# Optimization experiments

Measured on AMD Instinct MI355X. Metric: run time of the kernel, lower is better.

Reference implementation:

```python
import jax, jax.numpy as jnp
import numpy as np

# ---- constants from module defaults (n_transducers reduced 64->32) ----
ARC = 160          # transducer_arc_width
NTR = 32           # n_transducers
NMEAS = 256
NX = 360           # padded grid size
DX = 0.6
NSTEPS = 640       # nt
DT = 0.2
SIGMA = 12.0
TC = 3.2
FC = 1.0
NBC = 15
PAD = 73
C1, C2, C3 = -2.5, 4.0 / 3.0, -1.0 / 12.0

_thetas = np.linspace(0.0, 2.0 * np.pi, NMEAS + 1)[:-1]
_ti = np.floor(ARC * np.stack((np.cos(_thetas), np.sin(_thetas))) + (NX - 1) / 2).astype(np.int32)
MEAS_INDS = jnp.asarray(NX * _ti[0, :] + _ti[1, :])          # [256] flat grid indices
IN_INDS = MEAS_INDS[:: NMEAS // NTR]                         # [32] source-injection indices
_t = np.arange(NSTEPS) * DT
SOURCE = jnp.asarray((np.exp(-((_t - TC) ** 2) / (2.0 * SIGMA ** 2)) * np.sin(2.0 * np.pi * FC * _t)).astype(np.float32))


def get_abc(vp):
    # vp: [B, NX, NX] -> sponge damping profile, same overwrite order as torch code
    B = vp.shape[0]
    dimr = jnp.arange(NBC, dtype=vp.dtype)                   # [nbc]
    velmin = jnp.min(vp.reshape(B, -1), axis=-1)             # [B]
    a = (NBC - 1) * DX
    kappa = 3.0 * velmin * jnp.asarray(np.log(10000.0), vp.dtype) / (2.0 * a)
    d1 = kappa[:, None] * (dimr[None, :] * DX / a) ** 2      # [B, nbc]
    rev = d1[:, ::-1]
    damp = jnp.zeros_like(vp)
    damp = damp.at[:, :NBC, :].set(rev[:, :, None])
    damp = damp.at[:, -NBC:, :].set(d1[:, :, None])
    damp = damp.at[:, :, :NBC].set(rev[:, None, :])          # columns overwrite corners, as in torch
    damp = damp.at[:, :, -NBC:].set(d1[:, None, :])
    return damp


def _forward(v):
    v = jnp.pad(v[:, 0], ((0, 0), (PAD, PAD), (PAD, PAD)), constant_values=1.5)  # [B,360,360]
    B = v.shape[0]
    kappa = get_abc(v) * DT
    v2 = v * v
    alpha = v2 * (DT / DX) ** 2                              # [B,360,360]
    beta = (DT * DT) * v2.reshape(B, -1)[:, IN_INDS]         # [B,NTR]
    temp1 = 2.0 + 2.0 * C1 * alpha - kappa
    temp0 = 1.0 - kappa
    a_, t1_, t0_ = alpha[:, None], temp1[:, None], temp0[:, None]  # broadcast over transducer axis
    tx = jnp.arange(NTR)

    def step(carry, src_t):
        p0, p1 = carry                                        # each [B,NTR,360,360]
        lap = C2 * (jnp.roll(p1, 1, -2) + jnp.roll(p1, -1, -2) + jnp.roll(p1, 1, -1) + jnp.roll(p1, -1, -1)) \
            + C3 * (jnp.roll(p1, 2, -2) + jnp.roll(p1, -2, -2) + jnp.roll(p1, 2, -1) + jnp.roll(p1, -2, -1))
        p = a_ * lap + t1_ * p1 - t0_ * p0
        pf = p.reshape(B, NTR, NX * NX)
        pf = pf.at[:, tx, IN_INDS].add(beta * src_t)          # per-shot source injection
        m = pf[:, :, MEAS_INDS]                               # [B,NTR,NMEAS]
        return (p1, pf.reshape(B, NTR, NX, NX)), m

    z = jnp.zeros((B, NTR, NX, NX), dtype=v.dtype)
    _, meas = jax.lax.scan(step, (z, z), SOURCE)              # meas: [NSTEPS,B,NTR,NMEAS]
    return jnp.transpose(meas, (1, 2, 0, 3))                  # [B,NTR,NSTEPS,NMEAS]


def setup_inputs() -> dict:
    key = jax.random.key(0)
    v = jax.random.uniform(key, (1, 1, 214, 214), dtype=jnp.float32) + 1.0  # speeds ~[1,2]
    return {"v": v}


def reference(v):
    return _forward(v)
```

## Files before the change

kernel.cpp:

```cpp
#include <hip/hip_runtime.h>
#include <math.h>

#ifndef M_PI
#define M_PI 3.14159265358979323846
#endif

#define NXx   360
#define NXY   (NXx*NXx)
#define NTRc  32
#define NMEASc 256
#define NSTEPSc 640
#define NBCc  15
#define PADc  73
#define NVc   214

#define BROWS 45
#define NBANDS 8
#define NBLK  (NTRc*NBANDS)
#define NTHREADS 1024
#define NGrow (NXx/4)
#define GPB   (BROWS*NGrow)
#define NEDGE (4*NGrow)
#define LDSROWS 49
#define LDSFLOATS (2*LDSROWS*NXx)
#define NSLOT 4
#define HALO_PER (NSLOT*4*NXx)

#define C2f   1.3333334f
#define C3f  (-0.083333336f)
#define ADX2  0.11111111f
#define DT2f  0.04f
#define DTf   0.2f
#define DXf   0.6f

typedef float f32x4 __attribute__((ext_vector_type(4)));

__device__ __forceinline__ void store4_sys(float* p, float4 v) {
    f32x4 vv; vv.x = v.x; vv.y = v.y; vv.z = v.z; vv.w = v.w;
    asm volatile("global_store_dwordx4 %0, %1, off sc0 sc1" :: "v"(p), "v"(vv) : "memory");
}
__device__ __forceinline__ float4 load4_sys(const float* p) {
    f32x4 r;
    asm volatile("global_load_dwordx4 %0, %1, off sc0 sc1\n\ts_waitcnt vmcnt(0)"
                 : "=&v"(r) : "v"(p) : "memory");
    return make_float4(r.x, r.y, r.z, r.w);
}
__device__ __forceinline__ void storei_sys(int* p, int v) {
    asm volatile("global_store_dword %0, %1, off sc0 sc1" :: "v"(p), "v"(v) : "memory");
}
__device__ __forceinline__ int loadi_sys(const int* p) {
    int r;
    asm volatile("global_load_dword %0, %1, off sc0 sc1\n\ts_waitcnt vmcnt(0)"
                 : "=&v"(r) : "v"(p) : "memory");
    return r;
}
__device__ __forceinline__ void drain_vm() {
    asm volatile("s_waitcnt vmcnt(0)" ::: "memory");
}

__global__ void velmin_kernel(const float* __restrict__ v, float* __restrict__ velmin) {
    __shared__ float s[256];
    float m = 1.5f;
    for (int i = threadIdx.x; i < NVc*NVc; i += 256) m = fminf(m, v[i]);
    s[threadIdx.x] = m;
    __syncthreads();
    for (int o = 128; o > 0; o >>= 1) {
        if (threadIdx.x < o) s[threadIdx.x] = fminf(s[threadIdx.x], s[threadIdx.x+o]);
        __syncthreads();
    }
    if (threadIdx.x == 0) *velmin = s[0];
}

__global__ void coef_kernel(const float* __restrict__ v, const float* __restrict__ velmin_p,
                            float* __restrict__ alpha, float* __restrict__ kap) {
    int idx = blockIdx.x*256 + threadIdx.x;
    if (idx >= NXY) return;
    int i = idx / NXx, j = idx - i*NXx;
    float vc = 1.5f;
    if (i >= PADc && i < PADc+NVc && j >= PADc && j < PADc+NVc)
        vc = v[(i-PADc)*NVc + (j-PADc)];
    float v2 = vc*vc;
    float al = v2 * ADX2;
    float velmin = *velmin_p;
    const float a = (float)((NBCc-1)*0.6);
    float ks = 3.0f*velmin*9.2103405f/(2.0f*a);
    float damp = 0.0f;
    int k = -1;
    if (j >= NXx-NBCc)      k = j-(NXx-NBCc);
    else if (j < NBCc)      k = NBCc-1-j;
    else if (i >= NXx-NBCc) k = i-(NXx-NBCc);
    else if (i < NBCc)      k = NBCc-1-i;
    if (k >= 0) { float r = (float)k*DXf/a; damp = ks*r*r; }
    alpha[idx] = al;
    kap[idx]   = damp*DTf;
}

__global__ void beta_kernel(const float* __restrict__ v, const int* __restrict__ in_inds,
                            float* __restrict__ beta) {
    int tr = threadIdx.x;
    if (tr >= NTRc) return;
    int idx = in_inds[tr];
    int i = idx / NXx, j = idx - i*NXx;
    float vc = 1.5f;
    if (i >= PADc && i < PADc+NVc && j >= PADc && j < PADc+NVc)
        vc = v[(i-PADc)*NVc + (j-PADc)];
    beta[tr] = DT2f*vc*vc;
}

__global__ __launch_bounds__(NTHREADS, 4) void persist_kernel(
    const float* __restrict__ alpha, const float* __restrict__ kap,
    const float* __restrict__ beta, const float* __restrict__ src,
    const int* __restrict__ meas_inds, const int* __restrict__ in_inds,
    int* flags, float* haloG, float* __restrict__ out)
{
    extern __shared__ float lds[];
    const int tid  = threadIdx.x;
    const int b    = blockIdx.x;
    const int tr   = b >> 3, band = b & 7;
    const int band0 = band*BROWS;
    const int up = (tr<<3) | ((band+7)&7);
    const int dn = (tr<<3) | ((band+1)&7);

    float* buf0 = lds;
    float* buf1 = lds + LDSROWS*NXx;

    for (int i = tid; i < LDSFLOATS; i += NTHREADS) lds[i] = 0.0f;

    const float betaV = beta[tr];
    const int sCell = in_inds[tr];
    const int sr = sCell/NXx, sc = sCell - sr*NXx;

    int c0=-1,l0=0,r0=0,q0=-1; float4 A0=make_float4(0,0,0,0), K0=A0;
    int c1=-1,l1=0,r1=0,q1=-1; float4 A1=A0, K1=A0;
    int c2=-1,l2=0,r2=0,q2=-1; float4 A2=A0, K2=A0;
    int c3=-1,l3=0,r3=0,q3=-1; float4 A3=A0, K3=A0;
    int h0 = 0;

#define INIT_SLOT(KK, Ck,Lk,Rk,Qk,AAk,KKk) { \
    int gg = tid + KK*1024; \
    if (gg < GPB) { \
        int rloc, jg; \
        if (gg < NEDGE) { int kk = gg/NGrow; jg = gg - kk*NGrow; rloc = (kk<2)?kk:(41+kk); } \
        else { int ii = gg - NEDGE; rloc = 2 + ii/NGrow; jg = ii - (ii/NGrow)*NGrow; } \
        Ck = (rloc+2)*NGrow + jg; \
        Lk = Ck + ((jg==0)?NGrow-1:-1); \
        Rk = Ck + ((jg==NGrow-1)?-(NGrow-1):1); \
        int gr = band0 + rloc, gi = gr*NXx + jg*4; \
        AAk = *(const float4*)(alpha+gi); KKk = *(const float4*)(kap+gi); \
        Qk = (gr==sr && (sc>>2)==jg) ? (sc&3) : -1; \
    } }

    INIT_SLOT(0, c0,l0,r0,q0,A0,K0)
    INIT_SLOT(1, c1,l1,r1,q1,A1,K1)
    INIT_SLOT(2, c2,l2,r2,q2,A2,K2)
    INIT_SLOT(3, c3,l3,r3,q3,A3,K3)
#undef INIT_SLOT
    if (tid < NEDGE) {
        int kk = tid/NGrow, jg = tid - kk*NGrow;
        int rloc = (kk<2)?kk:(41+kk);
        int hrow = (rloc<2)? rloc : (rloc-41);
        h0 = hrow*NXx + jg*4;
    }

    bool mOwn = false; int mOff = 0;
    float* outP = out + ((size_t)tr*NSTEPSc)*NMEASc + tid;
    if (tid < NMEASc) {
        int mi = meas_inds[tid]; int row = mi/NXx, col = mi - row*NXx;
        if (row >= band0 && row < band0+BROWS) { mOwn = true; mOff = (row-band0+2)*NXx + col; }
    }

    float* myHalo = haloG + (size_t)b*HALO_PER;
    float* upHalo = haloG + (size_t)up*HALO_PER;
    float* dnHalo = haloG + (size_t)dn*HALO_PER;

    __syncthreads();

#define COMPUTE_PO(Ck,Lk,Rk,Qk,AAk,KKk) \
    float4 Cv = cur4[Ck], Lv = cur4[Lk], Rv = cur4[Rk]; \
    float4 U1 = cur4[Ck-NGrow], D1 = cur4[Ck+NGrow]; \
    float4 U2 = cur4[Ck-2*NGrow], D2 = cur4[Ck+2*NGrow]; \
    float4 Pp = nxt4[Ck]; float4 po; \
    { float lap = C2f*(U1.x+D1.x+Lv.w+Cv.y) + C3f*(U2.x+D2.x+Lv.z+Cv.z); \
      float t1v = 2.0f + 2.0f*(-2.5f)*AAk.x - KKk.x; float t0v = 1.0f - KKk.x; \
      po.x = AAk.x*lap + t1v*Cv.x - t0v*Pp.x; } \
    { float lap = C2f*(U1.y+D1.y+Cv.x+Cv.z) + C3f*(U2.y+D2.y+Lv.w+Cv.w); \
      float t1v = 2.0f + 2.0f*(-2.5f)*AAk.y - KKk.y; float t0v = 1.0f - KKk.y; \
      po.y = AAk.y*lap + t1v*Cv.y - t0v*Pp.y; } \
    { float lap = C2f*(U1.z+D1.z+Cv.y+Cv.w) + C3f*(U2.z+D2.z+Cv.x+Rv.x); \
      float t1v = 2.0f + 2.0f*(-2.5f)*AAk.z - KKk.z; float t0v = 1.0f - KKk.z; \
      po.z = AAk.z*lap + t1v*Cv.z - t0v*Pp.z; } \
    { float lap = C2f*(U1.w+D1.w+Cv.z+Rv.x) + C3f*(U2.w+D2.w+Cv.y+Rv.y); \
      float t1v = 2.0f + 2.0f*(-2.5f)*AAk.w - KKk.w; float t0v = 1.0f - KKk.w; \
      po.w = AAk.w*lap + t1v*Cv.w - t0v*Pp.w; } \
    if (Qk >= 0) { float add = betaV*srcT; \
        if (Qk==0) po.x += add; else if (Qk==1) po.y += add; \
        else if (Qk==2) po.z += add; else po.w += add; } \
    nxt4[Ck] = po;

    for (int t = 0; t < NSTEPSc; ++t) {
        const int slot = t & 1;
        const int hs   = (t+1) & 3;
        float* cur = (slot == 0) ? buf0 : buf1;
        float* nxt = (slot == 0) ? buf1 : buf0;
        const float4* cur4 = (const float4*)cur;
        float4* nxt4 = (float4*)nxt;
        const float srcT = src[t];

        if (tid < NEDGE) {
            COMPUTE_PO(c0,l0,r0,q0,A0,K0)
            store4_sys(myHalo + hs*4*NXx + h0, po);
            drain_vm();
        }
        __syncthreads();
        if (tid == 0) storei_sys(flags + b, t + 1);

        if (tid >= NEDGE) { COMPUTE_PO(c0,l0,r0,q0,A0,K0) }
        { COMPUTE_PO(c1,l1,r1,q1,A1,K1) }
        { COMPUTE_PO(c2,l2,r2,q2,A2,K2) }
        if (c3 >= 0) { COMPUTE_PO(c3,l3,r3,q3,A3,K3) }

        if (tid == 0) {
            int g = 0;
            while (loadi_sys(flags + up) <= t)
                { __builtin_amdgcn_s_sleep(1); if (++g > 200000) break; }
        }
        if (tid == 64) {
            int g = 0;
            while (loadi_sys(flags + dn) <= t)
                { __builtin_amdgcn_s_sleep(1); if (++g > 200000) break; }
        }
        __syncthreads();

        if (tid < 4*NGrow) {
            int rr = tid / NGrow, jg = tid - rr*NGrow;
            const float* sp = (rr < 2) ? (upHalo + (hs*4 + 2 + rr)*NXx + jg*4)
                                       : (dnHalo + (hs*4 + (rr-2))*NXx + jg*4);
            float4 hv = load4_sys(sp);
            int ldr = (rr < 2) ? rr : (45 + rr);
            *(float4*)(nxt + ldr*NXx + jg*4) = hv;
        }

        if (mOwn) outP[(size_t)t*NMEASc] = nxt[mOff];

        __syncthreads();
    }
#undef COMPUTE_PO
}

extern "C" void kernel_launch(void* const* d_in, const int* in_sizes, int n_in,
                              void* d_out, int out_size, void* d_ws, size_t ws_size,
                              hipStream_t stream) {
    const float* v = (const float*)d_in[0];
    float* out = (float*)d_out;

    float* haloG  = (float*)d_ws;
    float* alpha  = haloG + (size_t)NBLK*HALO_PER;
    float* kap    = alpha + NXY;
    float* beta   = kap + NXY;
    float* velmin = beta + NTRc;
    float* src_d  = velmin + 1;
    int*   meas_d = (int*)(src_d + NSTEPSc);
    int*   in_d   = meas_d + NMEASc;
    int*   flags  = in_d + NTRc;

    static int   h_tab[NMEASc + NTRc];
    static float h_src[NSTEPSc];
    {
        const double step = 2.0*M_PI/256.0;
        for (int k = 0; k < NMEASc; ++k) {
            double th = (double)k * step;
            int ti0 = (int)floor(160.0*cos(th) + 179.5);
            int ti1 = (int)floor(160.0*sin(th) + 179.5);
            h_tab[k] = NXx*ti0 + ti1;
        }
        for (int r = 0; r < NTRc; ++r) h_tab[NMEASc + r] = h_tab[r*(NMEASc/NTRc)];
        for (int t = 0; t < NSTEPSc; ++t) {
            double tt = (double)t * 0.2;
            double d  = tt - 3.2;
            double e  = exp(-(d*d) / 288.0);
            double s  = sin(6.283185307179586 * tt);
            h_src[t] = (float)(e * s);
        }
    }
    (void)hipMemcpyAsync(meas_d, h_tab, sizeof(int)*(NMEASc+NTRc), hipMemcpyHostToDevice, stream);
    (void)hipMemcpyAsync(src_d, h_src, sizeof(float)*NSTEPSc, hipMemcpyHostToDevice, stream);
    (void)hipMemsetAsync(haloG, 0, sizeof(float)*(size_t)NBLK*HALO_PER, stream);
    (void)hipMemsetAsync(flags, 0, sizeof(int)*NBLK, stream);

    velmin_kernel<<<1, 256, 0, stream>>>(v, velmin);
    coef_kernel<<<(NXY+255)/256, 256, 0, stream>>>(v, velmin, alpha, kap);
    beta_kernel<<<1, 64, 0, stream>>>(v, in_d, beta);

    (void)hipFuncSetAttribute((const void*)persist_kernel,
                        hipFuncAttributeMaxDynamicSharedMemorySize, LDSFLOATS*4);

    persist_kernel<<<NBLK, NTHREADS, LDSFLOATS*4, stream>>>(
        alpha, kap, beta, src_d, meas_d, in_d, flags, haloG, out);
}
```

Measured before the change: 2.248 ms.

## Assign each thread a 5-row vertical strip with register-rolled stencil reuse

Replaces the per-thread float4 slot assignment (up to 4 scattered cells per thread across 1024 threads) with 810 threads that each own a 5-row column strip. Vertical stencil neighbours are kept in a rolling register window, which cuts LDS reads per output. Edge strips (first and last) now compute 5 rows before the halo publish and barrier, where before only the 4 halo rows were computed there. This lengthens the critical section ahead of the flag signal. Block size drops to 832 threads, and each thread holds 10 float4 coefficient registers.

```diff
diff --git a/kernel.cpp b/kernel.cpp
--- a/kernel.cpp
+++ b/kernel.cpp
@@ -17,10 +17,9 @@
 #define BROWS 45
 #define NBANDS 8
 #define NBLK  (NTRc*NBANDS)
-#define NTHREADS 1024
+#define NTHREADS 832
 #define NGrow (NXx/4)
-#define GPB   (BROWS*NGrow)
-#define NEDGE (4*NGrow)
+#define NSTRIPT 810
 #define LDSROWS 49
 #define LDSFLOATS (2*LDSROWS*NXx)
 #define NSLOT 4
@@ -130,36 +129,29 @@
     const int sCell = in_inds[tr];
     const int sr = sCell/NXx, sc = sCell - sr*NXx;
 
-    int c0=-1,l0=0,r0=0,q0=-1; float4 A0=make_float4(0,0,0,0), K0=A0;
-    int c1=-1,l1=0,r1=0,q1=-1; float4 A1=A0, K1=A0;
-    int c2=-1,l2=0,r2=0,q2=-1; float4 A2=A0, K2=A0;
-    int c3=-1,l3=0,r3=0,q3=-1; float4 A3=A0, K3=A0;
-    int h0 = 0;
-
-#define INIT_SLOT(KK, Ck,Lk,Rk,Qk,AAk,KKk) { \
-    int gg = tid + KK*1024; \
-    if (gg < GPB) { \
-        int rloc, jg; \
-        if (gg < NEDGE) { int kk = gg/NGrow; jg = gg - kk*NGrow; rloc = (kk<2)?kk:(41+kk); } \
-        else { int ii = gg - NEDGE; rloc = 2 + ii/NGrow; jg = ii - (ii/NGrow)*NGrow; } \
-        Ck = (rloc+2)*NGrow + jg; \
-        Lk = Ck + ((jg==0)?NGrow-1:-1); \
-        Rk = Ck + ((jg==NGrow-1)?-(NGrow-1):1); \
-        int gr = band0 + rloc, gi = gr*NXx + jg*4; \
-        AAk = *(const float4*)(alpha+gi); KKk = *(const float4*)(kap+gi); \
-        Qk = (gr==sr && (sc>>2)==jg) ? (sc&3) : -1; \
-    } }
-
-    INIT_SLOT(0, c0,l0,r0,q0,A0,K0)
-    INIT_SLOT(1, c1,l1,r1,q1,A1,K1)
-    INIT_SLOT(2, c2,l2,r2,q2,A2,K2)
-    INIT_SLOT(3, c3,l3,r3,q3,A3,K3)
-#undef INIT_SLOT
-    if (tid < NEDGE) {
-        int kk = tid/NGrow, jg = tid - kk*NGrow;
-        int rloc = (kk<2)?kk:(41+kk);
-        int hrow = (rloc<2)? rloc : (rloc-41);
-        h0 = hrow*NXx + jg*4;
+    const bool isStrip = (tid < NSTRIPT);
+    const int s  = isStrip ? (tid/NGrow) : 0;
+    const int jg = isStrip ? (tid - s*NGrow) : 0;
+    const int r0 = 5*s;
+    const bool isEdge = isStrip && (s == 0 || s == 8);
+    const int jgm = (jg==0) ? NGrow-1 : jg-1;
+    const int jgp = (jg==NGrow-1) ? 0 : jg+1;
+
+    float4 Ar[5], Kr[5];
+    int qrow = -1, qcomp = 0;
+    if (isStrip) {
+#pragma unroll
+        for (int k = 0; k < 5; ++k) {
+            int gi = (band0 + r0 + k)*NXx + jg*4;
+            Ar[k] = *(const float4*)(alpha + gi);
+            Kr[k] = *(const float4*)(kap + gi);
+        }
+        if (sr >= band0+r0 && sr < band0+r0+5 && (sc>>2) == jg) {
+            qrow = sr - (band0+r0); qcomp = sc & 3;
+        }
+    } else {
+#pragma unroll
+        for (int k = 0; k < 5; ++k) { Ar[k] = make_float4(0,0,0,0); Kr[k] = Ar[k]; }
     }
 
     bool mOwn = false; int mOff = 0;
@@ -175,49 +167,64 @@
 
     __syncthreads();
 
-#define COMPUTE_PO(Ck,Lk,Rk,Qk,AAk,KKk) \
-    float4 Cv = cur4[Ck], Lv = cur4[Lk], Rv = cur4[Rk]; \
-    float4 U1 = cur4[Ck-NGrow], D1 = cur4[Ck+NGrow]; \
-    float4 U2 = cur4[Ck-2*NGrow], D2 = cur4[Ck+2*NGrow]; \
-    float4 Pp = nxt4[Ck]; float4 po; \
-    { float lap = C2f*(U1.x+D1.x+Lv.w+Cv.y) + C3f*(U2.x+D2.x+Lv.z+Cv.z); \
-      float t1v = 2.0f + 2.0f*(-2.5f)*AAk.x - KKk.x; float t0v = 1.0f - KKk.x; \
-      po.x = AAk.x*lap + t1v*Cv.x - t0v*Pp.x; } \
-    { float lap = C2f*(U1.y+D1.y+Cv.x+Cv.z) + C3f*(U2.y+D2.y+Lv.w+Cv.w); \
-      float t1v = 2.0f + 2.0f*(-2.5f)*AAk.y - KKk.y; float t0v = 1.0f - KKk.y; \
-      po.y = AAk.y*lap + t1v*Cv.y - t0v*Pp.y; } \
-    { float lap = C2f*(U1.z+D1.z+Cv.y+Cv.w) + C3f*(U2.z+D2.z+Cv.x+Rv.x); \
-      float t1v = 2.0f + 2.0f*(-2.5f)*AAk.z - KKk.z; float t0v = 1.0f - KKk.z; \
-      po.z = AAk.z*lap + t1v*Cv.z - t0v*Pp.z; } \
-    { float lap = C2f*(U1.w+D1.w+Cv.z+Rv.x) + C3f*(U2.w+D2.w+Cv.y+Rv.y); \
-      float t1v = 2.0f + 2.0f*(-2.5f)*AAk.w - KKk.w; float t0v = 1.0f - KKk.w; \
-      po.w = AAk.w*lap + t1v*Cv.w - t0v*Pp.w; } \
-    if (Qk >= 0) { float add = betaV*srcT; \
-        if (Qk==0) po.x += add; else if (Qk==1) po.y += add; \
-        else if (Qk==2) po.z += add; else po.w += add; } \
-    nxt4[Ck] = po;
+#define STRIP_COMPUTE(DOHALO) { \
+    const int base = r0*NGrow + jg; \
+    float4 cm2 = cur4[base]; \
+    float4 cm1 = cur4[base+NGrow]; \
+    float4 cc0 = cur4[base+2*NGrow]; \
+    float4 cp1 = cur4[base+3*NGrow]; \
+    float4 cp2 = cur4[base+4*NGrow]; \
+    _Pragma("unroll") \
+    for (int k = 0; k < 5; ++k) { \
+        const int ci = base + (2+k)*NGrow; \
+        float4 Lv = cur4[ci - jg + jgm]; \
+        float4 Rv = cur4[ci - jg + jgp]; \
+        float4 Pp = nxt4[ci]; \
+        float4 po; \
+        { float lap = C2f*(cm1.x+cp1.x+Lv.w+cc0.y) + C3f*(cm2.x+cp2.x+Lv.z+cc0.z); \
+          float t1v = 2.0f + 2.0f*(-2.5f)*Ar[k].x - Kr[k].x; float t0v = 1.0f - Kr[k].x; \
+          po.x = Ar[k].x*lap + t1v*cc0.x - t0v*Pp.x; } \
+        { float lap = C2f*(cm1.y+cp1.y+cc0.x+cc0.z) + C3f*(cm2.y+cp2.y+Lv.w+cc0.w); \
+          float t1v = 2.0f + 2.0f*(-2.5f)*Ar[k].y - Kr[k].y; float t0v = 1.0f - Kr[k].y; \
+          po.y = Ar[k].y*lap + t1v*cc0.y - t0v*Pp.y; } \
+        { float lap = C2f*(cm1.z+cp1.z+cc0.y+cc0.w) + C3f*(cm2.z+cp2.z+cc0.x+Rv.x); \
+          float t1v = 2.0f + 2.0f*(-2.5f)*Ar[k].z - Kr[k].z; float t0v = 1.0f - Kr[k].z; \
+          po.z = Ar[k].z*lap + t1v*cc0.z - t0v*Pp.z; } \
+        { float lap = C2f*(cm1.w+cp1.w+cc0.z+Rv.x) + C3f*(cm2.w+cp2.w+cc0.y+Rv.y); \
+          float t1v = 2.0f + 2.0f*(-2.5f)*Ar[k].w - Kr[k].w; float t0v = 1.0f - Kr[k].w; \
+          po.w = Ar[k].w*lap + t1v*cc0.w - t0v*Pp.w; } \
+        if (k == qrow) { float add = betaV*srcT; \
+            po.x += (qcomp==0)?add:0.0f; po.y += (qcomp==1)?add:0.0f; \
+            po.z += (qcomp==2)?add:0.0f; po.w += (qcomp==3)?add:0.0f; } \
+        nxt4[ci] = po; \
+        if (DOHALO) { \
+            if (s == 0 && k < 2) store4_sys(myHalo + hsOff + k*NXx + jg*4, po); \
+            if (s == 8 && k >= 3) store4_sys(myHalo + hsOff + (k-1)*NXx + jg*4, po); \
+        } \
+        cm2 = cm1; cm1 = cc0; cc0 = cp1; cp1 = cp2; \
+        if (k < 4) cp2 = cur4[base + (5+k)*NGrow]; \
+    } }
 
     for (int t = 0; t < NSTEPSc; ++t) {
         const int slot = t & 1;
         const int hs   = (t+1) & 3;
+        const int hsOff = hs*4*NXx;
         float* cur = (slot == 0) ? buf0 : buf1;
         float* nxt = (slot == 0) ? buf1 : buf0;
         const float4* cur4 = (const float4*)cur;
         float4* nxt4 = (float4*)nxt;
         const float srcT = src[t];
 
-        if (tid < NEDGE) {
-            COMPUTE_PO(c0,l0,r0,q0,A0,K0)
-            store4_sys(myHalo + hs*4*NXx + h0, po);
+        if (isEdge) {
+            STRIP_COMPUTE(1)
             drain_vm();
         }
         __syncthreads();
         if (tid == 0) storei_sys(flags + b, t + 1);
 
-        if (tid >= NEDGE) { COMPUTE_PO(c0,l0,r0,q0,A0,K0) }
-        { COMPUTE_PO(c1,l1,r1,q1,A1,K1) }
-        { COMPUTE_PO(c2,l2,r2,q2,A2,K2) }
-        if (c3 >= 0) { COMPUTE_PO(c3,l3,r3,q3,A3,K3) }
+        if (isStrip && !isEdge) {
+            STRIP_COMPUTE(0)
+        }
 
         if (tid == 0) {
             int g = 0;
@@ -232,19 +239,19 @@
         __syncthreads();
 
         if (tid < 4*NGrow) {
-            int rr = tid / NGrow, jg = tid - rr*NGrow;
-            const float* sp = (rr < 2) ? (upHalo + (hs*4 + 2 + rr)*NXx + jg*4)
-                                       : (dnHalo + (hs*4 + (rr-2))*NXx + jg*4);
+            int rr = tid / NGrow, jgq = tid - rr*NGrow;
+            const float* sp = (rr < 2) ? (upHalo + (hsOff + (2+rr)*NXx) + jgq*4)
+                                       : (dnHalo + (hsOff + (rr-2)*NXx) + jgq*4);
             float4 hv = load4_sys(sp);
             int ldr = (rr < 2) ? rr : (45 + rr);
-            *(float4*)(nxt + ldr*NXx + jg*4) = hv;
+            *(float4*)(nxt + ldr*NXx + jgq*4) = hv;
         }
 
         if (mOwn) outP[(size_t)t*NMEASc] = nxt[mOff];
 
         __syncthreads();
     }
-#undef COMPUTE_PO
+#undef STRIP_COMPUTE
 }
 
 extern "C" void kernel_launch(void* const* d_in, const int* in_sizes, int n_in,
```

Result: slower. 2.469 ms (+9.8%).

## Restructure step into warp-specialized strips with register-rolled rows and one barrier

Applied to the files above, without the earlier changes.

Interior rows are now computed by 720 threads, each walking a 5-row vertical strip and rotating the stencil's up/down rows through registers, which cuts repeated LDS reads. The alpha and kappa coefficients are reloaded from global memory every step instead of being held in registers. Two dedicated wavefronts poll the neighbour flags and copy the halo rows while the other threads compute. This removes one __syncthreads per step, and the measurement store is deferred to the next step. The trade-off is extra global traffic for the coefficients and a less balanced split of work across threads.

```diff
diff --git a/kernel.cpp b/kernel.cpp
--- a/kernel.cpp
+++ b/kernel.cpp
@@ -18,9 +18,7 @@
 #define NBANDS 8
 #define NBLK  (NTRc*NBANDS)
 #define NTHREADS 1024
-#define NGrow (NXx/4)
-#define GPB   (BROWS*NGrow)
-#define NEDGE (4*NGrow)
+#define NG    (NXx/4)
 #define LDSROWS 49
 #define LDSFLOATS (2*LDSROWS*NXx)
 #define NSLOT 4
@@ -128,45 +126,61 @@
 
     const float betaV = beta[tr];
     const int sCell = in_inds[tr];
-    const int sr = sCell/NXx, sc = sCell - sr*NXx;
-
-    int c0=-1,l0=0,r0=0,q0=-1; float4 A0=make_float4(0,0,0,0), K0=A0;
-    int c1=-1,l1=0,r1=0,q1=-1; float4 A1=A0, K1=A0;
-    int c2=-1,l2=0,r2=0,q2=-1; float4 A2=A0, K2=A0;
-    int c3=-1,l3=0,r3=0,q3=-1; float4 A3=A0, K3=A0;
-    int h0 = 0;
-
-#define INIT_SLOT(KK, Ck,Lk,Rk,Qk,AAk,KKk) { \
-    int gg = tid + KK*1024; \
-    if (gg < GPB) { \
-        int rloc, jg; \
-        if (gg < NEDGE) { int kk = gg/NGrow; jg = gg - kk*NGrow; rloc = (kk<2)?kk:(41+kk); } \
-        else { int ii = gg - NEDGE; rloc = 2 + ii/NGrow; jg = ii - (ii/NGrow)*NGrow; } \
-        Ck = (rloc+2)*NGrow + jg; \
-        Lk = Ck + ((jg==0)?NGrow-1:-1); \
-        Rk = Ck + ((jg==NGrow-1)?-(NGrow-1):1); \
-        int gr = band0 + rloc, gi = gr*NXx + jg*4; \
-        AAk = *(const float4*)(alpha+gi); KKk = *(const float4*)(kap+gi); \
-        Qk = (gr==sr && (sc>>2)==jg) ? (sc&3) : -1; \
-    } }
-
-    INIT_SLOT(0, c0,l0,r0,q0,A0,K0)
-    INIT_SLOT(1, c1,l1,r1,q1,A1,K1)
-    INIT_SLOT(2, c2,l2,r2,q2,A2,K2)
-    INIT_SLOT(3, c3,l3,r3,q3,A3,K3)
-#undef INIT_SLOT
-    if (tid < NEDGE) {
-        int kk = tid/NGrow, jg = tid - kk*NGrow;
-        int rloc = (kk<2)?kk:(41+kk);
-        int hrow = (rloc<2)? rloc : (rloc-41);
-        h0 = hrow*NXx + jg*4;
+    const int sr = sCell/NXx, scc = sCell - sr*NXx;
+    const int sb = sr - band0;
+    const int sq = scc >> 2, sqc = scc & 3;
+
+    const bool isEdgeT = (tid < 360);
+    int eCi = 0, eL = 0, eR = 0, eH = 0, eQ = -1;
+    float4 eA = make_float4(0,0,0,0), eK = eA;
+    if (isEdgeT) {
+        int kk = tid/NG, jg = tid - kk*NG;
+        int rowG = (kk < 2) ? kk : (41 + kk);
+        int ldsR = rowG + 2;
+        eCi = ldsR*NG + jg;
+        eL  = eCi - jg + ((jg==0) ? NG-1 : jg-1);
+        eR  = eCi - jg + ((jg==NG-1) ? 0 : jg+1);
+        eH  = kk*NXx + jg*4;
+        int gi = (band0 + rowG)*NXx + jg*4;
+        eA = *(const float4*)(alpha + gi);
+        eK = *(const float4*)(kap + gi);
+        eQ = (sb == rowG && sq == jg) ? sqc : -1;
+    }
+
+    const bool isStripT = (tid < 720);
+    int sBase = 0, sLo = 0, sRo = 0, sQk = -1;
+    const float* aP = alpha; const float* kP = kap;
+    if (isStripT) {
+        int ss = tid/NG, jg = tid - ss*NG;
+        sBase = (4 + 5*ss)*NG + jg;
+        sLo = (jg==0) ? NG-1 : -1;
+        sRo = (jg==NG-1) ? -(NG-1) : 1;
+        aP = alpha + (band0 + 2 + 5*ss)*NXx + jg*4;
+        kP = kap   + (band0 + 2 + 5*ss)*NXx + jg*4;
+        sQk = (sb >= 2+5*ss && sb < 7+5*ss && sq == jg) ? (sb - 2 - 5*ss) : -1;
+    }
+
+    const bool isFlatT = (tid >= 720 && tid < 810);
+    int fCi = 0, fL = 0, fR = 0, fQ = -1;
+    const float* aPf = alpha; const float* kPf = kap;
+    if (isFlatT) {
+        int jg = tid - 720;
+        fCi = 44*NG + jg;
+        fL  = fCi - jg + ((jg==0) ? NG-1 : jg-1);
+        fR  = fCi - jg + ((jg==NG-1) ? 0 : jg+1);
+        aPf = alpha + (band0 + 42)*NXx + jg*4;
+        kPf = kap   + (band0 + 42)*NXx + jg*4;
+        fQ = (sb == 42 && sq == jg) ? sqc : -1;
     }
 
     bool mOwn = false; int mOff = 0;
-    float* outP = out + ((size_t)tr*NSTEPSc)*NMEASc + tid;
+    float* outP = out;
     if (tid < NMEASc) {
         int mi = meas_inds[tid]; int row = mi/NXx, col = mi - row*NXx;
-        if (row >= band0 && row < band0+BROWS) { mOwn = true; mOff = (row-band0+2)*NXx + col; }
+        if (row >= band0 && row < band0+BROWS) {
+            mOwn = true; mOff = (row-band0+2)*NXx + col;
+            outP = out + ((size_t)tr*NSTEPSc)*NMEASc + tid;
+        }
     }
 
     float* myHalo = haloG + (size_t)b*HALO_PER;
@@ -175,76 +189,103 @@
 
     __syncthreads();
 
-#define COMPUTE_PO(Ck,Lk,Rk,Qk,AAk,KKk) \
-    float4 Cv = cur4[Ck], Lv = cur4[Lk], Rv = cur4[Rk]; \
-    float4 U1 = cur4[Ck-NGrow], D1 = cur4[Ck+NGrow]; \
-    float4 U2 = cur4[Ck-2*NGrow], D2 = cur4[Ck+2*NGrow]; \
-    float4 Pp = nxt4[Ck]; float4 po; \
+#define CELLMATH(Cv,U1,D1,U2,D2,Lv,Rv,Pp,AA,KK,QQ) \
+    float4 po; \
     { float lap = C2f*(U1.x+D1.x+Lv.w+Cv.y) + C3f*(U2.x+D2.x+Lv.z+Cv.z); \
-      float t1v = 2.0f + 2.0f*(-2.5f)*AAk.x - KKk.x; float t0v = 1.0f - KKk.x; \
-      po.x = AAk.x*lap + t1v*Cv.x - t0v*Pp.x; } \
+      float t1v = 2.0f + 2.0f*(-2.5f)*AA.x - KK.x; float t0v = 1.0f - KK.x; \
+      po.x = AA.x*lap + t1v*Cv.x - t0v*Pp.x; } \
     { float lap = C2f*(U1.y+D1.y+Cv.x+Cv.z) + C3f*(U2.y+D2.y+Lv.w+Cv.w); \
-      float t1v = 2.0f + 2.0f*(-2.5f)*AAk.y - KKk.y; float t0v = 1.0f - KKk.y; \
-      po.y = AAk.y*lap + t1v*Cv.y - t0v*Pp.y; } \
+      float t1v = 2.0f + 2.0f*(-2.5f)*AA.y - KK.y; float t0v = 1.0f - KK.y; \
+      po.y = AA.y*lap + t1v*Cv.y - t0v*Pp.y; } \
     { float lap = C2f*(U1.z+D1.z+Cv.y+Cv.w) + C3f*(U2.z+D2.z+Cv.x+Rv.x); \
-      float t1v = 2.0f + 2.0f*(-2.5f)*AAk.z - KKk.z; float t0v = 1.0f - KKk.z; \
-      po.z = AAk.z*lap + t1v*Cv.z - t0v*Pp.z; } \
+      float t1v = 2.0f + 2.0f*(-2.5f)*AA.z - KK.z; float t0v = 1.0f - KK.z; \
+      po.z = AA.z*lap + t1v*Cv.z - t0v*Pp.z; } \
     { float lap = C2f*(U1.w+D1.w+Cv.z+Rv.x) + C3f*(U2.w+D2.w+Cv.y+Rv.y); \
-      float t1v = 2.0f + 2.0f*(-2.5f)*AAk.w - KKk.w; float t0v = 1.0f - KKk.w; \
-      po.w = AAk.w*lap + t1v*Cv.w - t0v*Pp.w; } \
-    if (Qk >= 0) { float add = betaV*srcT; \
-        if (Qk==0) po.x += add; else if (Qk==1) po.y += add; \
-        else if (Qk==2) po.z += add; else po.w += add; } \
-    nxt4[Ck] = po;
+      float t1v = 2.0f + 2.0f*(-2.5f)*AA.w - KK.w; float t0v = 1.0f - KK.w; \
+      po.w = AA.w*lap + t1v*Cv.w - t0v*Pp.w; } \
+    if (QQ >= 0) { float add = betaV*srcT; \
+        po.x += (QQ==0)?add:0.0f; po.y += (QQ==1)?add:0.0f; \
+        po.z += (QQ==2)?add:0.0f; po.w += (QQ==3)?add:0.0f; }
 
     for (int t = 0; t < NSTEPSc; ++t) {
         const int slot = t & 1;
-        const int hs   = (t+1) & 3;
+        const int hsOff = ((t+1) & 3)*4*NXx;
         float* cur = (slot == 0) ? buf0 : buf1;
         float* nxt = (slot == 0) ? buf1 : buf0;
         const float4* cur4 = (const float4*)cur;
         float4* nxt4 = (float4*)nxt;
         const float srcT = src[t];
 
-        if (tid < NEDGE) {
-            COMPUTE_PO(c0,l0,r0,q0,A0,K0)
-            store4_sys(myHalo + hs*4*NXx + h0, po);
+        if (mOwn && t > 0) outP[(size_t)(t-1)*NMEASc] = cur[mOff];
+
+        if (isEdgeT) {
+            float4 Cv = cur4[eCi], Lv = cur4[eL], Rv = cur4[eR];
+            float4 U1 = cur4[eCi-NG], D1 = cur4[eCi+NG];
+            float4 U2 = cur4[eCi-2*NG], D2 = cur4[eCi+2*NG];
+            float4 Pp = nxt4[eCi];
+            CELLMATH(Cv,U1,D1,U2,D2,Lv,Rv,Pp,eA,eK,eQ)
+            nxt4[eCi] = po;
+            store4_sys(myHalo + hsOff + eH, po);
             drain_vm();
         }
         __syncthreads();
         if (tid == 0) storei_sys(flags + b, t + 1);
 
-        if (tid >= NEDGE) { COMPUTE_PO(c0,l0,r0,q0,A0,K0) }
-        { COMPUTE_PO(c1,l1,r1,q1,A1,K1) }
-        { COMPUTE_PO(c2,l2,r2,q2,A2,K2) }
-        if (c3 >= 0) { COMPUTE_PO(c3,l3,r3,q3,A3,K3) }
-
-        if (tid == 0) {
-            int g = 0;
-            while (loadi_sys(flags + up) <= t)
-                { __builtin_amdgcn_s_sleep(1); if (++g > 200000) break; }
-        }
-        if (tid == 64) {
-            int g = 0;
-            while (loadi_sys(flags + dn) <= t)
-                { __builtin_amdgcn_s_sleep(1); if (++g > 200000) break; }
-        }
+        if (isStripT) {
+            int ci = sBase;
+            float4 cm2 = cur4[ci-2*NG], cm1 = cur4[ci-NG], cc0 = cur4[ci];
+            float4 cp1 = cur4[ci+NG],  cp2 = cur4[ci+2*NG];
+#pragma unroll
+            for (int k = 0; k < 5; ++k) {
+                float4 Al = *(const float4*)(aP + k*NXx);
+                float4 Kp = *(const float4*)(kP + k*NXx);
+                float4 Lv = cur4[ci + sLo], Rv = cur4[ci + sRo];
+                float4 Pp = nxt4[ci];
+                CELLMATH(cc0,cm1,cp1,cm2,cp2,Lv,Rv,Pp,Al,Kp,(k==sQk?sqc:-1))
+                nxt4[ci] = po;
+                cm2 = cm1; cm1 = cc0; cc0 = cp1; cp1 = cp2;
+                if (k < 4) cp2 = cur4[ci + 3*NG];
+                ci += NG;
+            }
+        } else if (isFlatT) {
+            float4 Al = *(const float4*)(aPf);
+            float4 Kp = *(const float4*)(kPf);
+            float4 Cv = cur4[fCi], Lv = cur4[fL], Rv = cur4[fR];
+            float4 U1 = cur4[fCi-NG], D1 = cur4[fCi+NG];
+            float4 U2 = cur4[fCi-2*NG], D2 = cur4[fCi+2*NG];
+            float4 Pp = nxt4[fCi];
+            CELLMATH(Cv,U1,D1,U2,D2,Lv,Rv,Pp,Al,Kp,fQ)
+            nxt4[fCi] = po;
+        } else if (tid >= 832 && tid < 896) {
+            if (tid == 832) {
+                int g = 0;
+                while (loadi_sys(flags + up) <= t)
+                    { __builtin_amdgcn_s_sleep(1); if (++g > 2000000) break; }
+            }
+            int lane = tid - 832;
+            for (int i = lane; i < 2*NG; i += 64) {
+                int rr = (i < NG) ? 0 : 1, jq = i - rr*NG;
+                float4 hv = load4_sys(upHalo + hsOff + (2+rr)*NXx + jq*4);
+                *(float4*)(nxt + rr*NXx + jq*4) = hv;
+            }
+        } else if (tid >= 896 && tid < 960) {
+            if (tid == 896) {
+                int g = 0;
+                while (loadi_sys(flags + dn) <= t)
+                    { __builtin_amdgcn_s_sleep(1); if (++g > 2000000) break; }
+            }
+            int lane = tid - 896;
+            for (int i = lane; i < 2*NG; i += 64) {
+                int rr = (i < NG) ? 0 : 1, jq = i - rr*NG;
+                float4 hv = load4_sys(dnHalo + hsOff + rr*NXx + jq*4);
+                *(float4*)(nxt + (47+rr)*NXx + jq*4) = hv;
+            }
+        }
+
         __syncthreads();
-
-        if (tid < 4*NGrow) {
-            int rr = tid / NGrow, jg = tid - rr*NGrow;
-            const float* sp = (rr < 2) ? (upHalo + (hs*4 + 2 + rr)*NXx + jg*4)
-                                       : (dnHalo + (hs*4 + (rr-2))*NXx + jg*4);
-            float4 hv = load4_sys(sp);
-            int ldr = (rr < 2) ? rr : (45 + rr);
-            *(float4*)(nxt + ldr*NXx + jg*4) = hv;
-        }
-
-        if (mOwn) outP[(size_t)t*NMEASc] = nxt[mOff];
-
-        __syncthreads();
-    }
-#undef COMPUTE_PO
+    }
+    if (mOwn) outP[(size_t)(NSTEPSc-1)*NMEASc] = buf0[mOff];
+#undef CELLMATH
 }
 
 extern "C" void kernel_launch(void* const* d_in, const int* in_sizes, int n_in,
```

After: 2.826 ms. 1.26x slower.
